# Kernel optimization log

Measured on AMD Instinct MI355X. Metric: run time of the kernel, lower is better.

Reference implementation:

```python
import jax, jax.numpy as jnp
import numpy as np

N_TOKENS = 100000
EMB_DIM = 128
T_PERIOD = 48.0
N_BINS = 48
B, S = 64, 2048


def setup_inputs() -> dict:
    key = jax.random.key(0)
    k_t, k_tok, k_w = jax.random.split(key, 3)
    # times in [0, 48) -> T_mask all True, n == S (matches dynamic slice deterministically)
    times = jax.random.uniform(k_t, (B, S), dtype=jnp.float32) * T_PERIOD
    tokens = jax.random.randint(k_tok, (B, S), 0, N_TOKENS).astype(jnp.float32)
    X = jnp.stack([times, tokens], axis=-1)  # (B, S, 2)
    # variational embedding table: [mu | logvar], mu ~ truncnorm(-t, t), logvar = log(0.25)
    t = 1.0 / np.sqrt(N_TOKENS)
    mu = jnp.clip(jax.random.normal(k_w, (N_TOKENS, EMB_DIM), dtype=jnp.float32) * t, -t, t)
    logvar = jnp.full((N_TOKENS, EMB_DIM), np.log(0.25), dtype=jnp.float32)
    W = jnp.concatenate([mu, logvar], axis=1)  # (n_tokens, 2*emb_dim)
    return {"X": X, "W": W}


def reference(X, W):
    d = W.shape[1] // 2
    T = X[:, :, 0]                       # (B, S) event times
    tok = X[:, :, 1].astype(jnp.int32)   # (B, S) token ids
    T_mask = (T < T_PERIOD).astype(jnp.float32)

    e = W[tok]                           # (B, S, 2d) gather
    mu, logvar = e[..., :d], e[..., d:]
    # reparameterize (training mode): mu + std * eps, fixed noise key for determinism
    eps = jax.random.normal(jax.random.key(42), mu.shape, dtype=mu.dtype)
    emb = mu + jnp.exp(0.5 * logvar) * eps

    # KL(N(mu, var) || N(0, I)): mean over batch, sum over (seq, dim)
    kl_loss = 0.5 * jnp.sum(jnp.mean(-1.0 - logvar + mu * mu + jnp.exp(logvar), axis=0))

    # differential entropy per event, masked, cumulated and normalized to [0, 1]
    H = 0.5 * (d + d * jnp.log(2.0 * jnp.pi) + logvar.sum(axis=2)) * T_mask  # (B, S)
    H_cum = jnp.cumsum(H, axis=1)
    H_cum = H_cum / H_cum.max(axis=1, keepdims=True)

    # one-pass scatter-sum replacing the 48-iteration masked-sum loop:
    # event at position s goes to bin floor(H_cum * 48) iff 0 <= H_cum < 1
    bins = jnp.floor(H_cum * N_BINS).astype(jnp.int32)      # (B, S)
    valid = (H_cum >= 0.0) & (H_cum < 1.0)
    b_idx = jnp.arange(H_cum.shape[0], dtype=jnp.int32)[:, None]
    seg = jnp.where(valid, b_idx * N_BINS + bins, H_cum.shape[0] * N_BINS)
    out = jax.ops.segment_sum(
        emb.reshape(-1, d), seg.reshape(-1),
        num_segments=H_cum.shape[0] * N_BINS + 1,
    )[: H_cum.shape[0] * N_BINS].reshape(H_cum.shape[0], N_BINS, d)
    return out, kl_loss
```

## Files before the change

### kernel.cpp

```cpp
#include <hip/hip_runtime.h>
#include <stdint.h>
#include <math.h>

#define BB 64
#define SS 2048
#define DD 128
#define NB 48
#define NTOK 100000
#define HALF 8388608u
#define KL_OFF (BB*NB*DD)
#define WIN 8

__device__ __forceinline__ uint32_t rotl32(uint32_t x, uint32_t r){ return (x<<r)|(x>>(32u-r)); }

__device__ __forceinline__ uint2 threefry_0_42(uint32_t x0, uint32_t x1){
  const uint32_t ks0 = 0u, ks1 = 42u, ks2 = 0x1BD11BDAu ^ 0u ^ 42u;
  x0 += ks0; x1 += ks1;
#define TF_ROUND(r) { x0 += x1; x1 = rotl32(x1, r); x1 ^= x0; }
  TF_ROUND(13u) TF_ROUND(15u) TF_ROUND(26u) TF_ROUND(6u)
  x0 += ks1; x1 += ks2 + 1u;
  TF_ROUND(17u) TF_ROUND(29u) TF_ROUND(16u) TF_ROUND(24u)
  x0 += ks2; x1 += ks0 + 2u;
  TF_ROUND(13u) TF_ROUND(15u) TF_ROUND(26u) TF_ROUND(6u)
  x0 += ks0; x1 += ks1 + 3u;
  TF_ROUND(17u) TF_ROUND(29u) TF_ROUND(16u) TF_ROUND(24u)
  x0 += ks1; x1 += ks2 + 4u;
  TF_ROUND(13u) TF_ROUND(15u) TF_ROUND(26u) TF_ROUND(6u)
  x0 += ks2; x1 += ks0 + 5u;
#undef TF_ROUND
  return make_uint2(x0, x1);
}

__device__ __forceinline__ float fast_erfinv(float x){
  float w = -__logf(__fmaf_rn(x, -x, 1.0f));
  bool c = w < 5.0f;
  float t = c ? (w - 2.5f) : (__builtin_amdgcn_sqrtf(w) - 3.0f);
  float p =              c ? 2.81022636e-08f : -0.000200214257f;
  p = __fmaf_rn(p, t,    c ? 3.43273939e-07f : 0.000100950558f);
  p = __fmaf_rn(p, t,    c ? -3.5233877e-06f : 0.00134934322f);
  p = __fmaf_rn(p, t,    c ? -4.39150654e-06f : -0.00367342844f);
  p = __fmaf_rn(p, t,    c ? 0.00021858087f  : 0.00573950773f);
  p = __fmaf_rn(p, t,    c ? -0.00125372503f : -0.0076224613f);
  p = __fmaf_rn(p, t,    c ? -0.00417768164f : 0.00943887047f);
  p = __fmaf_rn(p, t,    c ? 0.246640727f    : 1.00167406f);
  p = __fmaf_rn(p, t,    c ? 1.50140941f     : 2.83297682f);
  return p * x;
}

__device__ __forceinline__ float jax_normal_from_bits(uint32_t bits){
  float f   = __uint_as_float((bits >> 9) | 0x3F800000u);
  float u01 = f - 1.0f;
  const float lo = __uint_as_float(0xBF7FFFFFu);
  float u = fmaxf(lo, __fmaf_rn(u01, 2.0f, lo));
  return 1.41421356237f * fast_erfinv(u);
}

__global__ __launch_bounds__(256) void k_prep(const float4* __restrict__ W4,
                                              float* __restrict__ lsum,
                                              float* __restrict__ g){
  __shared__ float mu_s[8][128];
  __shared__ float lv_s[8][128];
  __shared__ float gpart[8][32];
  __shared__ float apart[8][8];
  int t = threadIdx.x;
  int blk = blockIdx.x;
  #pragma unroll
  for (int h=0; h<2; h++){
    int q = h*256 + t;
    int r = q >> 6, c = q & 63;
    float4 v = W4[(size_t)blk*512 + q];
    if (c < 32) ((float4*)mu_s[r])[c]      = v;
    else        ((float4*)lv_s[r])[c - 32] = v;
  }
  __syncthreads();
  {
    int tl = t>>5, i = t&31;
    float gp = 0.f;
    #pragma unroll
    for (int c=0;c<4;c++){
      int d = i + 32*c;
      float mu = mu_s[tl][d], lv = lv_s[tl][d];
      gp += (-1.0f - lv) + mu*mu + __expf(lv);
    }
    gpart[tl][i] = gp;
  }
  if (t < 64){
    int tl = t>>3, j = t&7;
    float a = lv_s[tl][j];
    #pragma unroll
    for (int k=1;k<16;k++) a = __fadd_rn(a, lv_s[tl][8*k+j]);
    apart[tl][j] = a;
  }
  __syncthreads();
  if (t < 8){
    const float* p = apart[t];
    float s01 = __fadd_rn(p[0],p[1]);
    float s23 = __fadd_rn(p[2],p[3]);
    float s45 = __fadd_rn(p[4],p[5]);
    float s67 = __fadd_rn(p[6],p[7]);
    lsum[blk*8 + t] = __fadd_rn(__fadd_rn(s01,s23), __fadd_rn(s45,s67));
    float gs = 0.f;
    #pragma unroll
    for (int i=0;i<32;i++) gs += gpart[t][i];
    g[blk*8 + t] = gs;
  }
}

__global__ __launch_bounds__(1024) void k_bins(const float* __restrict__ X, const float* __restrict__ lsum,
                                               const float* __restrict__ g,
                                               int8_t* __restrict__ bins, float* __restrict__ out){
  __shared__ float buf[4096];
  __shared__ float redm[16];
  __shared__ float redk[16];
  int b = blockIdx.x, t = threadIdx.x;
  float twopi_f = (float)(2.0 * M_PI);
  float L = (float)log((double)twopi_f);
  float C1 = __fadd_rn(128.0f, __fmul_rn(128.0f, L));
  float klacc = 0.f;
  for (int s=t; s<SS; s+=1024){
    float T    = X[(b*SS+s)*2 + 0];
    int   tok  = (int)X[(b*SS+s)*2 + 1];
    float ls   = lsum[tok];
    klacc     += g[tok];
    float h    = __fmul_rn(0.5f, __fadd_rn(C1, ls));
    float mask = (T < 48.0f) ? 1.0f : 0.0f;
    buf[s] = __fmul_rn(h, mask);
  }
  __syncthreads();
  {
    int offL = 0, sz = SS;
    for (int lev=0; lev<11; lev++){
      int n = sz >> 1; int offN = offL + sz;
      for (int k=t; k<n; k+=1024)
        buf[offN + k] = __fadd_rn(buf[offL + 2*k], buf[offL + 2*k + 1]);
      __syncthreads();
      offL = offN; sz = n;
    }
  }
  for (int lev=10; lev>=0; lev--){
    int offC = 4096 - (4096 >> lev);
    int offN = 4096 - (4096 >> (lev+1));
    int half = (2048 >> lev) >> 1;
    for (int k=t; k<half; k+=1024){
      float odd  = buf[offN + k];
      float even = (k == 0) ? buf[offC] : __fadd_rn(buf[offN + k - 1], buf[offC + 2*k]);
      buf[offC + 2*k]     = even;
      buf[offC + 2*k + 1] = odd;
    }
    __syncthreads();
  }
  float m = fmaxf(buf[t], buf[t + 1024]);
  #pragma unroll
  for (int o=32; o>0; o>>=1) m = fmaxf(m, __shfl_down(m, o));
  if ((t & 63) == 0) redm[t >> 6] = m;
  __syncthreads();
  float maxv = redm[0];
  #pragma unroll
  for (int i=1;i<16;i++) maxv = fmaxf(maxv, redm[i]);
  for (int s=t; s<SS; s+=1024){
    float norm = __fdiv_rn(buf[s], maxv);
    int bin = (int)floorf(__fmul_rn(norm, 48.0f));
    bool valid = (norm >= 0.0f) && (norm < 1.0f);
    bins[b*SS + s] = valid ? (int8_t)bin : (int8_t)(-1);
  }
  #pragma unroll
  for (int o=32; o>0; o>>=1) klacc += __shfl_down(klacc, o);
  if ((t & 63) == 0) redk[t >> 6] = klacc;
  __syncthreads();
  if (t == 0){
    float s = 0.f;
    #pragma unroll
    for (int i=0;i<16;i++) s += redk[i];
    atomicAdd(&out[KL_OFF], s * (0.5f/64.0f));
  }
}

__global__ __launch_bounds__(256, 8) void k_accum(const float* __restrict__ X, const float* __restrict__ W,
                                                  const int8_t* __restrict__ bins,
                                                  float* __restrict__ out){
  __shared__ float acc[2*WIN*DD];
  __shared__ int   tok_s[2][32];
  __shared__ int   bin_s[2][32];
  __shared__ int   hi_s[2];
  int t = threadIdx.x;
  int bp = blockIdx.x >> 6;
  int chunk = blockIdx.x & 63;
  int sub = t >> 7, lane = t & 127;
  for (int i=t; i<2*WIN*DD; i+=256) acc[i] = 0.f;
  if (t < 128){
    int r = (t >> 5) & 1, i = t & 31;
    int row = bp + r*32;
    if (t < 64) tok_s[r][i] = (int)X[(row*SS + chunk*32 + i)*2 + 1];
    else        bin_s[r][i] = (int)bins[row*SS + chunk*32 + i];
  }
  __syncthreads();
  if (t < 2){
    int h = -1;
    for (int i=0;i<32;i++) h = max(h, bin_s[t][i]);
    hi_s[t] = h;
  }
  int base0 = bin_s[0][0], base1 = bin_s[1][0];
  int tk0 = tok_s[0][sub], tk1 = tok_s[1][sub];
  float mu0 = W[tk0*256 + lane], lv0 = W[tk0*256 + 128 + lane];
  float mu1 = W[tk1*256 + lane], lv1 = W[tk1*256 + 128 + lane];
  int cur0 = -1, cur1 = -1;
  float r0 = 0.f, r1 = 0.f;
  for (int it=0; it<16; it++){
    float mu0n=0.f, lv0n=0.f, mu1n=0.f, lv1n=0.f;
    if (it < 15){
      int sln = (it+1)*2 + sub;
      int a0 = tok_s[0][sln], a1 = tok_s[1][sln];
      mu0n = W[a0*256 + lane]; lv0n = W[a0*256 + 128 + lane];
      mu1n = W[a1*256 + lane]; lv1n = W[a1*256 + 128 + lane];
    }
    int sl = it*2 + sub;
    int s = chunk*32 + sl;
    uint32_t i32 = (uint32_t)(bp*SS + s) * 128u + (uint32_t)lane;
    uint2 rr = threefry_0_42(i32, i32 + HALF);
    float e0 = __fmaf_rn(__expf(0.5f*lv0), jax_normal_from_bits(rr.x), mu0);
    float e1 = __fmaf_rn(__expf(0.5f*lv1), jax_normal_from_bits(rr.y), mu1);
    int b0 = bin_s[0][sl];
    int b1 = bin_s[1][sl];
    if (b0 != cur0){
      if (cur0 >= 0){
        int o = cur0 - base0;
        if (o < WIN) atomicAdd(&acc[o*DD + lane], r0);
        else atomicAdd(&out[(bp*NB + cur0)*DD + lane], r0);
      }
      cur0 = b0; r0 = 0.f;
    }
    if (b0 >= 0) r0 += e0;
    if (b1 != cur1){
      if (cur1 >= 0){
        int o = cur1 - base1;
        if (o < WIN) atomicAdd(&acc[WIN*DD + o*DD + lane], r1);
        else atomicAdd(&out[((bp+32)*NB + cur1)*DD + lane], r1);
      }
      cur1 = b1; r1 = 0.f;
    }
    if (b1 >= 0) r1 += e1;
    mu0=mu0n; lv0=lv0n; mu1=mu1n; lv1=lv1n;
  }
  if (cur0 >= 0){
    int o = cur0 - base0;
    if (o < WIN) atomicAdd(&acc[o*DD + lane], r0);
    else atomicAdd(&out[(bp*NB + cur0)*DD + lane], r0);
  }
  if (cur1 >= 0){
    int o = cur1 - base1;
    if (o < WIN) atomicAdd(&acc[WIN*DD + o*DD + lane], r1);
    else atomicAdd(&out[((bp+32)*NB + cur1)*DD + lane], r1);
  }
  __syncthreads();
  int hi0 = hi_s[0], hi1 = hi_s[1];
  int top0 = min(hi0, base0 + WIN - 1);
  if (base0 >= 0 && top0 >= base0){
    int total = (top0 - base0 + 1)*DD;
    for (int q=t; q<total; q+=256){
      int o = q >> 7, dim = q & 127;
      atomicAdd(&out[(bp*NB + base0 + o)*DD + dim], acc[o*DD + dim]);
    }
  }
  int top1 = min(hi1, base1 + WIN - 1);
  if (base1 >= 0 && top1 >= base1){
    int total = (top1 - base1 + 1)*DD;
    for (int q=t; q<total; q+=256){
      int o = q >> 7, dim = q & 127;
      atomicAdd(&out[((bp+32)*NB + base1 + o)*DD + dim], acc[WIN*DD + o*DD + dim]);
    }
  }
}

extern "C" void kernel_launch(void* const* d_in, const int* in_sizes, int n_in,
                              void* d_out, int out_size, void* d_ws, size_t ws_size,
                              hipStream_t stream){
  const float* X = (const float*)d_in[0];
  const float* W = (const float*)d_in[1];
  float* out  = (float*)d_out;
  float* lsum = (float*)d_ws;
  float* g    = (float*)((char*)d_ws + 400000);
  int8_t* bins = (int8_t*)((char*)d_ws + 800000);
  (void)in_sizes; (void)n_in; (void)ws_size;
  hipMemsetAsync(d_out, 0, (size_t)out_size*sizeof(float), stream);
  k_prep <<<NTOK/8, 256, 0, stream>>>((const float4*)W, lsum, g);
  k_bins <<<BB,    1024, 0, stream>>>(X, lsum, g, bins, out);
  k_accum<<<2048,   256, 0, stream>>>(X, W, bins, out);
}
```

Measured before the change: 208.4 us.

## Split bin kernel into wide gather pass and scan pass; deepen accum prefetch

Moves the random lsum/g gathers and the KL reduction out of the 64-block scan kernel into a separate 256-block kernel that writes per-event entropies to a workspace buffer, so the latency-bound gathers are spread over more CUs. The scan kernel then only reads contiguous entropies. k_accum is unrolled by two with a two-deep register prefetch of W rows to hide more gather latency. The cost is an extra kernel launch, an extra global round trip for hbuf, and higher register pressure in k_accum.

```diff
diff --git a/kernel.cpp b/kernel.cpp
--- a/kernel.cpp
+++ b/kernel.cpp
@@ -106,26 +106,42 @@
   }
 }
 
-__global__ __launch_bounds__(1024) void k_bins(const float* __restrict__ X, const float* __restrict__ lsum,
-                                               const float* __restrict__ g,
-                                               int8_t* __restrict__ bins, float* __restrict__ out){
-  __shared__ float buf[4096];
-  __shared__ float redm[16];
-  __shared__ float redk[16];
-  int b = blockIdx.x, t = threadIdx.x;
+__global__ __launch_bounds__(256) void k_h(const float* __restrict__ X,
+                                           const float* __restrict__ lsum,
+                                           const float* __restrict__ g,
+                                           float* __restrict__ hbuf,
+                                           float* __restrict__ out){
+  __shared__ float redk[4];
+  int t = threadIdx.x;
   float twopi_f = (float)(2.0 * M_PI);
   float L = (float)log((double)twopi_f);
   float C1 = __fadd_rn(128.0f, __fmul_rn(128.0f, L));
   float klacc = 0.f;
-  for (int s=t; s<SS; s+=1024){
-    float T    = X[(b*SS+s)*2 + 0];
-    int   tok  = (int)X[(b*SS+s)*2 + 1];
-    float ls   = lsum[tok];
-    klacc     += g[tok];
-    float h    = __fmul_rn(0.5f, __fadd_rn(C1, ls));
+  #pragma unroll
+  for (int k=0; k<2; k++){
+    int i = blockIdx.x*512 + k*256 + t;
+    float T   = X[i*2 + 0];
+    int  tok  = (int)X[i*2 + 1];
+    float ls  = lsum[tok];
+    klacc    += g[tok];
+    float h   = __fmul_rn(0.5f, __fadd_rn(C1, ls));
     float mask = (T < 48.0f) ? 1.0f : 0.0f;
-    buf[s] = __fmul_rn(h, mask);
-  }
+    hbuf[i] = __fmul_rn(h, mask);
+  }
+  #pragma unroll
+  for (int o=32; o>0; o>>=1) klacc += __shfl_down(klacc, o);
+  if ((t & 63) == 0) redk[t >> 6] = klacc;
+  __syncthreads();
+  if (t == 0)
+    atomicAdd(&out[KL_OFF], (redk[0]+redk[1]+redk[2]+redk[3]) * (0.5f/64.0f));
+}
+
+__global__ __launch_bounds__(1024) void k_scan(const float* __restrict__ hbuf,
+                                               int8_t* __restrict__ bins){
+  __shared__ float buf[4096];
+  __shared__ float redm[16];
+  int b = blockIdx.x, t = threadIdx.x;
+  for (int s=t; s<SS; s+=1024) buf[s] = hbuf[b*SS + s];
   __syncthreads();
   {
     int offL = 0, sz = SS;
@@ -163,17 +179,37 @@
     bool valid = (norm >= 0.0f) && (norm < 1.0f);
     bins[b*SS + s] = valid ? (int8_t)bin : (int8_t)(-1);
   }
-  #pragma unroll
-  for (int o=32; o>0; o>>=1) klacc += __shfl_down(klacc, o);
-  if ((t & 63) == 0) redk[t >> 6] = klacc;
-  __syncthreads();
-  if (t == 0){
-    float s = 0.f;
-    #pragma unroll
-    for (int i=0;i<16;i++) s += redk[i];
-    atomicAdd(&out[KL_OFF], s * (0.5f/64.0f));
-  }
-}
+}
+
+#define K2_BODY(SLOT, MU0, LV0, MU1, LV1)                                     \
+  {                                                                           \
+    int sl = (SLOT);                                                          \
+    int s = chunk*32 + sl;                                                    \
+    uint32_t i32 = (uint32_t)(bp*SS + s) * 128u + (uint32_t)lane;             \
+    uint2 rr = threefry_0_42(i32, i32 + HALF);                                \
+    float e0 = __fmaf_rn(__expf(0.5f*(LV0)), jax_normal_from_bits(rr.x), (MU0)); \
+    float e1 = __fmaf_rn(__expf(0.5f*(LV1)), jax_normal_from_bits(rr.y), (MU1)); \
+    int b0 = bin_s[0][sl];                                                    \
+    int b1 = bin_s[1][sl];                                                    \
+    if (b0 != cur0){                                                          \
+      if (cur0 >= 0){                                                         \
+        int o = cur0 - base0;                                                 \
+        if (o < WIN) atomicAdd(&acc[o*DD + lane], r0);                        \
+        else atomicAdd(&out[(bp*NB + cur0)*DD + lane], r0);                   \
+      }                                                                       \
+      cur0 = b0; r0 = 0.f;                                                    \
+    }                                                                         \
+    if (b0 >= 0) r0 += e0;                                                    \
+    if (b1 != cur1){                                                          \
+      if (cur1 >= 0){                                                         \
+        int o = cur1 - base1;                                                 \
+        if (o < WIN) atomicAdd(&acc[WIN*DD + o*DD + lane], r1);               \
+        else atomicAdd(&out[((bp+32)*NB + cur1)*DD + lane], r1);              \
+      }                                                                       \
+      cur1 = b1; r1 = 0.f;                                                    \
+    }                                                                         \
+    if (b1 >= 0) r1 += e1;                                                    \
+  }
 
 __global__ __launch_bounds__(256, 8) void k_accum(const float* __restrict__ X, const float* __restrict__ W,
                                                   const int8_t* __restrict__ bins,
@@ -200,46 +236,38 @@
     hi_s[t] = h;
   }
   int base0 = bin_s[0][0], base1 = bin_s[1][0];
-  int tk0 = tok_s[0][sub], tk1 = tok_s[1][sub];
-  float mu0 = W[tk0*256 + lane], lv0 = W[tk0*256 + 128 + lane];
-  float mu1 = W[tk1*256 + lane], lv1 = W[tk1*256 + 128 + lane];
+  float mu0A, lv0A, mu1A, lv1A, mu0B, lv0B, mu1B, lv1B;
+  {
+    int a0 = tok_s[0][sub], a1 = tok_s[1][sub];
+    mu0A = W[a0*256 + lane]; lv0A = W[a0*256 + 128 + lane];
+    mu1A = W[a1*256 + lane]; lv1A = W[a1*256 + 128 + lane];
+  }
+  {
+    int a0 = tok_s[0][2+sub], a1 = tok_s[1][2+sub];
+    mu0B = W[a0*256 + lane]; lv0B = W[a0*256 + 128 + lane];
+    mu1B = W[a1*256 + lane]; lv1B = W[a1*256 + 128 + lane];
+  }
   int cur0 = -1, cur1 = -1;
   float r0 = 0.f, r1 = 0.f;
-  for (int it=0; it<16; it++){
-    float mu0n=0.f, lv0n=0.f, mu1n=0.f, lv1n=0.f;
-    if (it < 15){
-      int sln = (it+1)*2 + sub;
-      int a0 = tok_s[0][sln], a1 = tok_s[1][sln];
-      mu0n = W[a0*256 + lane]; lv0n = W[a0*256 + 128 + lane];
-      mu1n = W[a1*256 + lane]; lv1n = W[a1*256 + 128 + lane];
-    }
-    int sl = it*2 + sub;
-    int s = chunk*32 + sl;
-    uint32_t i32 = (uint32_t)(bp*SS + s) * 128u + (uint32_t)lane;
-    uint2 rr = threefry_0_42(i32, i32 + HALF);
-    float e0 = __fmaf_rn(__expf(0.5f*lv0), jax_normal_from_bits(rr.x), mu0);
-    float e1 = __fmaf_rn(__expf(0.5f*lv1), jax_normal_from_bits(rr.y), mu1);
-    int b0 = bin_s[0][sl];
-    int b1 = bin_s[1][sl];
-    if (b0 != cur0){
-      if (cur0 >= 0){
-        int o = cur0 - base0;
-        if (o < WIN) atomicAdd(&acc[o*DD + lane], r0);
-        else atomicAdd(&out[(bp*NB + cur0)*DD + lane], r0);
-      }
-      cur0 = b0; r0 = 0.f;
-    }
-    if (b0 >= 0) r0 += e0;
-    if (b1 != cur1){
-      if (cur1 >= 0){
-        int o = cur1 - base1;
-        if (o < WIN) atomicAdd(&acc[WIN*DD + o*DD + lane], r1);
-        else atomicAdd(&out[((bp+32)*NB + cur1)*DD + lane], r1);
-      }
-      cur1 = b1; r1 = 0.f;
-    }
-    if (b1 >= 0) r1 += e1;
-    mu0=mu0n; lv0=lv0n; mu1=mu1n; lv1=lv1n;
+  for (int it=0; it<16; it+=2){
+    float n0=0.f, n1=0.f, n2=0.f, n3=0.f;
+    if (it+2 < 16){
+      int sl = (it+2)*2 + sub;
+      int a0 = tok_s[0][sl], a1 = tok_s[1][sl];
+      n0 = W[a0*256 + lane]; n1 = W[a0*256 + 128 + lane];
+      n2 = W[a1*256 + lane]; n3 = W[a1*256 + 128 + lane];
+    }
+    K2_BODY(it*2 + sub, mu0A, lv0A, mu1A, lv1A)
+    mu0A = n0; lv0A = n1; mu1A = n2; lv1A = n3;
+    float m0=0.f, m1=0.f, m2=0.f, m3=0.f;
+    if (it+3 < 16){
+      int sl = (it+3)*2 + sub;
+      int a0 = tok_s[0][sl], a1 = tok_s[1][sl];
+      m0 = W[a0*256 + lane]; m1 = W[a0*256 + 128 + lane];
+      m2 = W[a1*256 + lane]; m3 = W[a1*256 + 128 + lane];
+    }
+    K2_BODY((it+1)*2 + sub, mu0B, lv0B, mu1B, lv1B)
+    mu0B = m0; lv0B = m1; mu1B = m2; lv1B = m3;
   }
   if (cur0 >= 0){
     int o = cur0 - base0;
@@ -280,9 +308,11 @@
   float* lsum = (float*)d_ws;
   float* g    = (float*)((char*)d_ws + 400000);
   int8_t* bins = (int8_t*)((char*)d_ws + 800000);
+  float* hbuf = (float*)((char*)d_ws + 931072);
   (void)in_sizes; (void)n_in; (void)ws_size;
   hipMemsetAsync(d_out, 0, (size_t)out_size*sizeof(float), stream);
   k_prep <<<NTOK/8, 256, 0, stream>>>((const float4*)W, lsum, g);
-  k_bins <<<BB,    1024, 0, stream>>>(X, lsum, g, bins, out);
+  k_h    <<<256,    256, 0, stream>>>(X, lsum, g, hbuf, out);
+  k_scan <<<BB,    1024, 0, stream>>>(hbuf, bins);
   k_accum<<<2048,   256, 0, stream>>>(X, W, bins, out);
 }
```

After: 221.2 us. 1.06x slower.
